# Performance work log

Measured on AMD Instinct MI355X. Metric: run time of the kernel, lower is better.

The kernel has to match this reference:

```python
import jax, jax.numpy as jnp
import numpy as np

B, S, D = 4, 2048, 1024
H = 16
DK = D // H  # 64


def setup_inputs() -> dict:
    key = jax.random.key(0)
    k1, k2, k3 = jax.random.split(key, 3)
    std_qkv = (2.0 / (D + 3 * D)) ** 0.5
    std_o = (2.0 / (D + D)) ** 0.5
    x = jax.random.normal(k1, (B, S, D), dtype=jnp.float32)
    W_qkv = jax.random.normal(k2, (3 * D, D), dtype=jnp.float32) * std_qkv
    W_o = jax.random.normal(k3, (D, D), dtype=jnp.float32) * std_o
    return {"x": x, "W_qkv": W_qkv, "W_o": W_o}


def reference(x, W_qkv, W_o):
    b, s, d = x.shape
    # qkv projection: [b, s, 3*H*DK]
    qkv = jnp.einsum('bsd,ed->bse', x, W_qkv)
    # rearrange '(c h dk)' -> c, b, h, s, dk
    qkv = qkv.reshape(b, s, 3, H, DK)
    qkv = jnp.transpose(qkv, (2, 0, 3, 1, 4))  # [3, b, h, s, dk]
    q, k, v = qkv[0], qkv[1], qkv[2]
    # scaled dot product attention with causal mask
    scores = jnp.einsum('bhqd,bhkd->bhqk', q, k) / (DK ** 0.5)
    causal = jnp.tril(jnp.ones((s, s), dtype=bool))
    scores = jnp.where(causal, scores, -jnp.inf)
    probs = jax.nn.softmax(scores, axis=-1)
    heads = jnp.einsum('bhqk,bhkd->bhqd', probs, v)
    # merge heads: [b, s, H*DK]
    heads = jnp.transpose(heads, (0, 2, 1, 3)).reshape(b, s, H * DK)
    return jnp.einsum('bse,de->bsd', heads, W_o)
```

## Files before the change

kernel.cpp:

```cpp
#include <hip/hip_runtime.h>
#include <hip/hip_bf16.h>

#define BB 4
#define SS 2048
#define DD 1024
#define HH 16
#define DKK 64

typedef __bf16 bf16x8 __attribute__((ext_vector_type(8)));
typedef float floatx4 __attribute__((ext_vector_type(4)));

#if __has_builtin(__builtin_amdgcn_exp2f)
#define EXP2(x) __builtin_amdgcn_exp2f(x)
#else
#define EXP2(x) exp2f(x)
#endif

__device__ __forceinline__ float b2f(unsigned short u) {
    union { unsigned int i; float f; } c;
    c.i = ((unsigned int)u) << 16;
    return c.f;
}
__device__ __forceinline__ unsigned short f2b(float f) {
    unsigned int i = __float_as_uint(f);
    unsigned int r = (i + 0x7FFFu + ((i >> 16) & 1u)) >> 16;
    return (unsigned short)r;
}
__device__ __forceinline__ unsigned int pkpair(float a, float b) {
    unsigned int ia = (__float_as_uint(a) + 0x8000u) >> 16;
    unsigned int ib = (__float_as_uint(b) + 0x8000u) & 0xffff0000u;
    return ia | ib;
}

__device__ __forceinline__ void gload_lds16(const unsigned short* g,
                                            unsigned short* l) {
    __builtin_amdgcn_global_load_lds(
        (const __attribute__((address_space(1))) unsigned int*)g,
        (__attribute__((address_space(3))) unsigned int*)l, 16, 0, 0);
}

__global__ void cvt_f32_bf16(const float* __restrict__ in,
                             unsigned short* __restrict__ out, int n4) {
    int i = blockIdx.x * blockDim.x + threadIdx.x;
    if (i >= n4) return;
    float4 v = ((const float4*)in)[i];
    ushort4 o;
    o.x = f2b(v.x); o.y = f2b(v.y); o.z = f2b(v.z); o.w = f2b(v.w);
    ((ushort4*)out)[i] = o;
}

template <typename CT>
__global__ void gemm_nt_lds(const unsigned short* __restrict__ A,
                            const unsigned short* __restrict__ B,
                            CT* __restrict__ C, int M, int N, int K) {
    __shared__ unsigned short Alds[128][32];
    __shared__ unsigned short Blds[128][32];

    const int tid  = threadIdx.x;
    const int lane = tid & 63;
    const int w    = tid >> 6;
    const int wm   = (w & 1) * 64;
    const int wn   = (w >> 1) * 64;

    const int m0 = blockIdx.x * 128;
    const int n0 = blockIdx.y * 128;

    const int row16 = lane & 15;
    const int part  = lane >> 4;
    const int rbase = part * 4;

    const int srow = lane >> 2;
    const int scol = (lane & 3) * 8;

    const unsigned short* Ag = A + (size_t)(m0 + w * 16 + srow) * K + scol;
    const unsigned short* Bg = B + (size_t)(n0 + w * 16 + srow) * K + scol;
    unsigned short* Al = &Alds[w * 16][0];
    unsigned short* Bl = &Blds[w * 16][0];
    const size_t rstep = (size_t)64 * K;

    floatx4 acc[4][4] = {};

    for (int k0 = 0; k0 < K; k0 += 32) {
        __syncthreads();
        gload_lds16(Ag + k0,         Al);
        gload_lds16(Ag + rstep + k0, Al + 64 * 32);
        gload_lds16(Bg + k0,         Bl);
        gload_lds16(Bg + rstep + k0, Bl + 64 * 32);
        __syncthreads();

        bf16x8 af[4], bfr[4];
#pragma unroll
        for (int i = 0; i < 4; ++i)
            af[i] = *(const bf16x8*)&Alds[wm + i * 16 + row16][part * 8];
#pragma unroll
        for (int j = 0; j < 4; ++j)
            bfr[j] = *(const bf16x8*)&Blds[wn + j * 16 + row16][part * 8];
#pragma unroll
        for (int i = 0; i < 4; ++i)
#pragma unroll
            for (int j = 0; j < 4; ++j)
                acc[i][j] = __builtin_amdgcn_mfma_f32_16x16x32_bf16(
                    af[i], bfr[j], acc[i][j], 0, 0, 0);
    }

#pragma unroll
    for (int i = 0; i < 4; ++i) {
#pragma unroll
        for (int j = 0; j < 4; ++j) {
            const int row = m0 + wm + i * 16 + rbase;
            const int col = n0 + wn + j * 16 + row16;
#pragma unroll
            for (int r = 0; r < 4; ++r) {
                size_t idx = (size_t)(row + r) * N + col;
                if constexpr (sizeof(CT) == 2) C[idx] = f2b(acc[i][j][r]);
                else                           C[idx] = acc[i][j][r];
            }
        }
    }
}

__global__ void repack_kv(const unsigned short* __restrict__ qkv,
                          unsigned short* __restrict__ Kp,
                          unsigned short* __restrict__ Vt) {
    __shared__ unsigned short Vs[64][72];
    const int st = blockIdx.x, h = blockIdx.y, b = blockIdx.z;
    const int tid = threadIdx.x;
    const size_t base = ((size_t)((b * HH + h) * (SS / 64) + st)) * 4096;

#pragma unroll
    for (int p = 0; p < 2; ++p) {
        const int row = p * 32 + (tid >> 3);
        const int chunk = tid & 7;
        size_t src = (size_t)(b * SS + st * 64 + row) * (3 * DD) +
                     DD + h * DKK + chunk * 8;
        uint4 kv = *(const uint4*)(qkv + src);
        *(uint4*)(Kp + base + (chunk >> 2) * 2048 + row * 32 + (chunk & 3) * 8) = kv;
        uint4 vv = *(const uint4*)(qkv + src + DD);
        *(uint4*)&Vs[row][chunk * 8] = vv;
    }
    __syncthreads();
#pragma unroll
    for (int p = 0; p < 2; ++p) {
        const int dk = p * 32 + (tid >> 3);
        const int s8 = tid & 7;
        union { unsigned short u[8]; uint4 v; } pk;
#pragma unroll
        for (int j = 0; j < 8; ++j) pk.u[j] = Vs[s8 * 8 + j][dk];
        *(uint4*)(Vt + base + (s8 >> 2) * 2048 + dk * 32 + (s8 & 3) * 8) = pk.v;
    }
}

struct StripState {
    bf16x8 qf[2][2];
    floatx4 O[2][4];
    float mrow[2], lrow[2];
    int q0w;
};

__device__ __forceinline__ void strip_init(
    StripState& S, const unsigned short* __restrict__ qkv,
    int b, int h, int q0w, int row16, int part) {
    const float c1 = 0.180336884f;
    S.q0w = q0w;
#pragma unroll
    for (int qt = 0; qt < 2; ++qt) {
        S.mrow[qt] = -1e30f;
        S.lrow[qt] = 0.f;
#pragma unroll
        for (int dt = 0; dt < 4; ++dt) S.O[qt][dt] = floatx4{0, 0, 0, 0};
#pragma unroll
        for (int u = 0; u < 2; ++u) {
            const unsigned short* qp = qkv +
                (size_t)(b * SS + q0w + qt * 16 + row16) * (3 * DD) +
                h * DKK + u * 32 + part * 8;
            union { uint4 r; unsigned short us[8]; } raw;
            raw.r = *(const uint4*)qp;
            union { unsigned short us[8]; bf16x8 v; } sq;
#pragma unroll
            for (int j = 0; j < 8; ++j) sq.us[j] = f2b(b2f(raw.us[j]) * c1);
            S.qf[qt][u] = sq.v;
        }
    }
}

__device__ __forceinline__ void strip_tile(
    StripState& S, int k0, const bf16x8 kf[2][4], const bf16x8 vf[2][4],
    int row16, int part, int rbase) {
#pragma unroll
    for (int qt = 0; qt < 2; ++qt) {
        floatx4 sc[4] = {};
#pragma unroll
        for (int u = 0; u < 2; ++u)
#pragma unroll
            for (int kt = 0; kt < 4; ++kt)
                sc[kt] = __builtin_amdgcn_mfma_f32_16x16x32_bf16(
                    kf[u][kt], S.qf[qt][u], sc[kt], 0, 0, 0);

        const int qa = S.q0w + qt * 16 + row16;
        const bool full = (k0 + 63 <= S.q0w + qt * 16);
        float mx = -1e30f;
#pragma unroll
        for (int kt = 0; kt < 4; ++kt)
#pragma unroll
            for (int r = 0; r < 4; ++r) {
                float s = sc[kt][r];
                if (!full) {
                    int ka = k0 + kt * 16 + rbase + r;
                    s = (ka <= qa) ? s : -1e30f;
                }
                sc[kt][r] = s;
                mx = fmaxf(mx, s);
            }
        mx = fmaxf(mx, __shfl_xor(mx, 16));
        mx = fmaxf(mx, __shfl_xor(mx, 32));
        float mnew = fmaxf(S.mrow[qt], mx);
        float alpha = EXP2(S.mrow[qt] - mnew);

        float ps = 0.f;
        unsigned int pk[4][2];
#pragma unroll
        for (int kt = 0; kt < 4; ++kt) {
            float e0 = EXP2(sc[kt][0] - mnew);
            float e1 = EXP2(sc[kt][1] - mnew);
            float e2 = EXP2(sc[kt][2] - mnew);
            float e3 = EXP2(sc[kt][3] - mnew);
            ps += (e0 + e1) + (e2 + e3);
            pk[kt][0] = pkpair(e0, e1);
            pk[kt][1] = pkpair(e2, e3);
        }
        ps += __shfl_xor(ps, 16);
        ps += __shfl_xor(ps, 32);
        S.lrow[qt] = S.lrow[qt] * alpha + ps;
        S.mrow[qt] = mnew;

#pragma unroll
        for (int dt = 0; dt < 4; ++dt) S.O[qt][dt] *= alpha;

        const int l0 = row16 + ((part & 1) * 2 + 0) * 16;
        const int l1 = row16 + ((part & 1) * 2 + 1) * 16;
        const bool hi = (part >> 1);
#pragma unroll
        for (int u = 0; u < 2; ++u) {
            unsigned int lo00 = (unsigned int)__shfl((int)pk[2 * u][0], l0);
            unsigned int lo01 = (unsigned int)__shfl((int)pk[2 * u][1], l0);
            unsigned int lo10 = (unsigned int)__shfl((int)pk[2 * u][0], l1);
            unsigned int lo11 = (unsigned int)__shfl((int)pk[2 * u][1], l1);
            unsigned int hi00 = (unsigned int)__shfl((int)pk[2 * u + 1][0], l0);
            unsigned int hi01 = (unsigned int)__shfl((int)pk[2 * u + 1][1], l0);
            unsigned int hi10 = (unsigned int)__shfl((int)pk[2 * u + 1][0], l1);
            unsigned int hi11 = (unsigned int)__shfl((int)pk[2 * u + 1][1], l1);
            union { unsigned int u32[4]; bf16x8 v; } P;
            P.u32[0] = hi ? hi00 : lo00;
            P.u32[1] = hi ? hi01 : lo01;
            P.u32[2] = hi ? hi10 : lo10;
            P.u32[3] = hi ? hi11 : lo11;
#pragma unroll
            for (int dt = 0; dt < 4; ++dt)
                S.O[qt][dt] = __builtin_amdgcn_mfma_f32_16x16x32_bf16(
                    vf[u][dt], P.v, S.O[qt][dt], 0, 0, 0);
        }
    }
}

__device__ __forceinline__ void strip_store(
    StripState& S, unsigned short* __restrict__ heads,
    int b, int h, int row16, int rbase) {
#pragma unroll
    for (int qt = 0; qt < 2; ++qt) {
        float inv = 1.f / S.lrow[qt];
#pragma unroll
        for (int dt = 0; dt < 4; ++dt) {
            ushort4 o4;
            o4.x = f2b(S.O[qt][dt][0] * inv);
            o4.y = f2b(S.O[qt][dt][1] * inv);
            o4.z = f2b(S.O[qt][dt][2] * inv);
            o4.w = f2b(S.O[qt][dt][3] * inv);
            size_t base = (size_t)(b * SS + S.q0w + qt * 16 + row16) * DD +
                          h * DKK + dt * 16 + rbase;
            *(ushort4*)&heads[base] = o4;
        }
    }
}

__global__ __launch_bounds__(256, 2) void attn_mfma6(
    const unsigned short* __restrict__ qkv,
    const unsigned short* __restrict__ Kp,
    const unsigned short* __restrict__ Vt,
    unsigned short* __restrict__ heads) {
    const int tid  = threadIdx.x;
    const int lane = tid & 63;
    const int w    = tid >> 6;

    const int bx   = blockIdx.x;
    const int xcd  = bx & 7;
    const int slot = bx >> 3;
    const int pair = xcd * 8 + (slot >> 3);
    const int blk  = slot & 7;
    const int b = pair >> 4, h = pair & 15;

    const int jA = blk * 4 + w;
    const int jB = 63 - jA;
    const int ntA = jA / 2 + 1;
    const int ntB = jB / 2 + 1;

    const int row16 = lane & 15;
    const int part  = lane >> 4;
    const int rbase = part * 4;

    StripState SA, SB;
    strip_init(SA, qkv, b, h, jA * 32, row16, part);
    strip_init(SB, qkv, b, h, jB * 32, row16, part);

    const size_t tb = (size_t)pair * (SS / 64) * 4096;

    for (int t = 0; t < ntB; ++t) {
        const int k0 = t * 64;
        const unsigned short* kbase = Kp + tb + (size_t)t * 4096;
        const unsigned short* vbase = Vt + tb + (size_t)t * 4096;
        bf16x8 kf[2][4], vf[2][4];
#pragma unroll
        for (int u = 0; u < 2; ++u)
#pragma unroll
            for (int i = 0; i < 4; ++i) {
                kf[u][i] = *(const bf16x8*)(kbase + u * 2048 +
                                            (i * 16 + row16) * 32 + part * 8);
                vf[u][i] = *(const bf16x8*)(vbase + u * 2048 +
                                            (i * 16 + row16) * 32 + part * 8);
            }
        strip_tile(SB, k0, kf, vf, row16, part, rbase);
        if (t < ntA) strip_tile(SA, k0, kf, vf, row16, part, rbase);
    }

    strip_store(SA, heads, b, h, row16, rbase);
    strip_store(SB, heads, b, h, row16, rbase);
}

extern "C" void kernel_launch(void* const* d_in, const int* in_sizes, int n_in,
                              void* d_out, int out_size, void* d_ws,
                              size_t ws_size, hipStream_t stream) {
    const float* x    = (const float*)d_in[0];
    const float* Wqkv = (const float*)d_in[1];
    const float* Wo   = (const float*)d_in[2];
    float* out = (float*)d_out;

    const size_t NX  = (size_t)BB * SS * DD;
    const size_t NWQ = (size_t)3 * DD * DD;
    const size_t NWO = (size_t)DD * DD;
    const size_t NKV = (size_t)BB * HH * SS * DKK;

    unsigned short* xb     = (unsigned short*)d_ws;
    unsigned short* wqkvb  = xb + NX;
    unsigned short* wob    = wqkvb + NWQ;
    unsigned short* qkvb   = wob + NWO;
    unsigned short* headsb = qkvb + (size_t)BB * SS * 3 * DD;
    unsigned short* Kp     = headsb + NX;
    unsigned short* Vtp    = Kp + NKV;

    cvt_f32_bf16<<<(int)(NX / 4 / 256), 256, 0, stream>>>(x, xb, (int)(NX / 4));
    cvt_f32_bf16<<<(int)(NWQ / 4 / 256), 256, 0, stream>>>(Wqkv, wqkvb, (int)(NWQ / 4));
    cvt_f32_bf16<<<(int)(NWO / 4 / 256), 256, 0, stream>>>(Wo, wob, (int)(NWO / 4));

    gemm_nt_lds<unsigned short><<<dim3(BB * SS / 128, 3 * DD / 128), 256, 0,
                                  stream>>>(xb, wqkvb, qkvb, BB * SS, 3 * DD, DD);

    repack_kv<<<dim3(SS / 64, HH, BB), 256, 0, stream>>>(qkvb, Kp, Vtp);

    attn_mfma6<<<dim3(512), 256, 0, stream>>>(qkvb, Kp, Vtp, headsb);

    gemm_nt_lds<float><<<dim3(BB * SS / 128, DD / 128), 256, 0, stream>>>(
        headsb, wob, out, BB * SS, DD, DD);
}
```

Before: 267.7 us.

## Shrink attention query strips to 16 rows and double block count

Each wave now handles two 16-row query strips instead of two 32-row strips, so the attention kernel launches 1024 blocks rather than 512 and the launch bounds allow 4 blocks per CU. Register pressure per wave drops, which is meant to raise occupancy and improve load balance across CUs. The cost is that each K/V fragment loaded from global memory now feeds half as many query rows, so K/V read traffic per unit of work doubles.

```diff
diff --git a/kernel.cpp b/kernel.cpp
--- a/kernel.cpp
+++ b/kernel.cpp
@@ -151,9 +151,9 @@
 }
 
 struct StripState {
-    bf16x8 qf[2][2];
-    floatx4 O[2][4];
-    float mrow[2], lrow[2];
+    bf16x8 qf[2];
+    floatx4 O[4];
+    float mrow, lrow;
     int q0w;
 };
 
@@ -162,127 +162,118 @@
     int b, int h, int q0w, int row16, int part) {
     const float c1 = 0.180336884f;
     S.q0w = q0w;
-#pragma unroll
-    for (int qt = 0; qt < 2; ++qt) {
-        S.mrow[qt] = -1e30f;
-        S.lrow[qt] = 0.f;
-#pragma unroll
-        for (int dt = 0; dt < 4; ++dt) S.O[qt][dt] = floatx4{0, 0, 0, 0};
-#pragma unroll
-        for (int u = 0; u < 2; ++u) {
-            const unsigned short* qp = qkv +
-                (size_t)(b * SS + q0w + qt * 16 + row16) * (3 * DD) +
-                h * DKK + u * 32 + part * 8;
-            union { uint4 r; unsigned short us[8]; } raw;
-            raw.r = *(const uint4*)qp;
-            union { unsigned short us[8]; bf16x8 v; } sq;
-#pragma unroll
-            for (int j = 0; j < 8; ++j) sq.us[j] = f2b(b2f(raw.us[j]) * c1);
-            S.qf[qt][u] = sq.v;
-        }
+    S.mrow = -1e30f;
+    S.lrow = 0.f;
+#pragma unroll
+    for (int dt = 0; dt < 4; ++dt) S.O[dt] = floatx4{0, 0, 0, 0};
+#pragma unroll
+    for (int u = 0; u < 2; ++u) {
+        const unsigned short* qp = qkv +
+            (size_t)(b * SS + q0w + row16) * (3 * DD) +
+            h * DKK + u * 32 + part * 8;
+        union { uint4 r; unsigned short us[8]; } raw;
+        raw.r = *(const uint4*)qp;
+        union { unsigned short us[8]; bf16x8 v; } sq;
+#pragma unroll
+        for (int j = 0; j < 8; ++j) sq.us[j] = f2b(b2f(raw.us[j]) * c1);
+        S.qf[u] = sq.v;
     }
 }
 
 __device__ __forceinline__ void strip_tile(
     StripState& S, int k0, const bf16x8 kf[2][4], const bf16x8 vf[2][4],
     int row16, int part, int rbase) {
-#pragma unroll
-    for (int qt = 0; qt < 2; ++qt) {
-        floatx4 sc[4] = {};
-#pragma unroll
-        for (int u = 0; u < 2; ++u)
-#pragma unroll
-            for (int kt = 0; kt < 4; ++kt)
-                sc[kt] = __builtin_amdgcn_mfma_f32_16x16x32_bf16(
-                    kf[u][kt], S.qf[qt][u], sc[kt], 0, 0, 0);
-
-        const int qa = S.q0w + qt * 16 + row16;
-        const bool full = (k0 + 63 <= S.q0w + qt * 16);
-        float mx = -1e30f;
+    floatx4 sc[4] = {};
+#pragma unroll
+    for (int u = 0; u < 2; ++u)
 #pragma unroll
         for (int kt = 0; kt < 4; ++kt)
-#pragma unroll
-            for (int r = 0; r < 4; ++r) {
-                float s = sc[kt][r];
-                if (!full) {
-                    int ka = k0 + kt * 16 + rbase + r;
-                    s = (ka <= qa) ? s : -1e30f;
-                }
-                sc[kt][r] = s;
-                mx = fmaxf(mx, s);
+            sc[kt] = __builtin_amdgcn_mfma_f32_16x16x32_bf16(
+                kf[u][kt], S.qf[u], sc[kt], 0, 0, 0);
+
+    const int qa = S.q0w + row16;
+    const bool full = (k0 + 63 <= S.q0w);
+    float mx = -1e30f;
+#pragma unroll
+    for (int kt = 0; kt < 4; ++kt)
+#pragma unroll
+        for (int r = 0; r < 4; ++r) {
+            float s = sc[kt][r];
+            if (!full) {
+                int ka = k0 + kt * 16 + rbase + r;
+                s = (ka <= qa) ? s : -1e30f;
             }
-        mx = fmaxf(mx, __shfl_xor(mx, 16));
-        mx = fmaxf(mx, __shfl_xor(mx, 32));
-        float mnew = fmaxf(S.mrow[qt], mx);
-        float alpha = EXP2(S.mrow[qt] - mnew);
-
-        float ps = 0.f;
-        unsigned int pk[4][2];
-#pragma unroll
-        for (int kt = 0; kt < 4; ++kt) {
-            float e0 = EXP2(sc[kt][0] - mnew);
-            float e1 = EXP2(sc[kt][1] - mnew);
-            float e2 = EXP2(sc[kt][2] - mnew);
-            float e3 = EXP2(sc[kt][3] - mnew);
-            ps += (e0 + e1) + (e2 + e3);
-            pk[kt][0] = pkpair(e0, e1);
-            pk[kt][1] = pkpair(e2, e3);
+            sc[kt][r] = s;
+            mx = fmaxf(mx, s);
         }
-        ps += __shfl_xor(ps, 16);
-        ps += __shfl_xor(ps, 32);
-        S.lrow[qt] = S.lrow[qt] * alpha + ps;
-        S.mrow[qt] = mnew;
-
-#pragma unroll
-        for (int dt = 0; dt < 4; ++dt) S.O[qt][dt] *= alpha;
-
-        const int l0 = row16 + ((part & 1) * 2 + 0) * 16;
-        const int l1 = row16 + ((part & 1) * 2 + 1) * 16;
-        const bool hi = (part >> 1);
-#pragma unroll
-        for (int u = 0; u < 2; ++u) {
-            unsigned int lo00 = (unsigned int)__shfl((int)pk[2 * u][0], l0);
-            unsigned int lo01 = (unsigned int)__shfl((int)pk[2 * u][1], l0);
-            unsigned int lo10 = (unsigned int)__shfl((int)pk[2 * u][0], l1);
-            unsigned int lo11 = (unsigned int)__shfl((int)pk[2 * u][1], l1);
-            unsigned int hi00 = (unsigned int)__shfl((int)pk[2 * u + 1][0], l0);
-            unsigned int hi01 = (unsigned int)__shfl((int)pk[2 * u + 1][1], l0);
-            unsigned int hi10 = (unsigned int)__shfl((int)pk[2 * u + 1][0], l1);
-            unsigned int hi11 = (unsigned int)__shfl((int)pk[2 * u + 1][1], l1);
-            union { unsigned int u32[4]; bf16x8 v; } P;
-            P.u32[0] = hi ? hi00 : lo00;
-            P.u32[1] = hi ? hi01 : lo01;
-            P.u32[2] = hi ? hi10 : lo10;
-            P.u32[3] = hi ? hi11 : lo11;
-#pragma unroll
-            for (int dt = 0; dt < 4; ++dt)
-                S.O[qt][dt] = __builtin_amdgcn_mfma_f32_16x16x32_bf16(
-                    vf[u][dt], P.v, S.O[qt][dt], 0, 0, 0);
-        }
+    mx = fmaxf(mx, __shfl_xor(mx, 16));
+    mx = fmaxf(mx, __shfl_xor(mx, 32));
+    float mnew = fmaxf(S.mrow, mx);
+    float alpha = EXP2(S.mrow - mnew);
+
+    float ps = 0.f;
+    unsigned int pk[4][2];
+#pragma unroll
+    for (int kt = 0; kt < 4; ++kt) {
+        float e0 = EXP2(sc[kt][0] - mnew);
+        float e1 = EXP2(sc[kt][1] - mnew);
+        float e2 = EXP2(sc[kt][2] - mnew);
+        float e3 = EXP2(sc[kt][3] - mnew);
+        ps += (e0 + e1) + (e2 + e3);
+        pk[kt][0] = pkpair(e0, e1);
+        pk[kt][1] = pkpair(e2, e3);
+    }
+    ps += __shfl_xor(ps, 16);
+    ps += __shfl_xor(ps, 32);
+    S.lrow = S.lrow * alpha + ps;
+    S.mrow = mnew;
+
+#pragma unroll
+    for (int dt = 0; dt < 4; ++dt) S.O[dt] *= alpha;
+
+    const int l0 = row16 + ((part & 1) * 2 + 0) * 16;
+    const int l1 = row16 + ((part & 1) * 2 + 1) * 16;
+    const bool hi = (part >> 1);
+#pragma unroll
+    for (int u = 0; u < 2; ++u) {
+        unsigned int lo00 = (unsigned int)__shfl((int)pk[2 * u][0], l0);
+        unsigned int lo01 = (unsigned int)__shfl((int)pk[2 * u][1], l0);
+        unsigned int lo10 = (unsigned int)__shfl((int)pk[2 * u][0], l1);
+        unsigned int lo11 = (unsigned int)__shfl((int)pk[2 * u][1], l1);
+        unsigned int hi00 = (unsigned int)__shfl((int)pk[2 * u + 1][0], l0);
+        unsigned int hi01 = (unsigned int)__shfl((int)pk[2 * u + 1][1], l0);
+        unsigned int hi10 = (unsigned int)__shfl((int)pk[2 * u + 1][0], l1);
+        unsigned int hi11 = (unsigned int)__shfl((int)pk[2 * u + 1][1], l1);
+        union { unsigned int u32[4]; bf16x8 v; } P;
+        P.u32[0] = hi ? hi00 : lo00;
+        P.u32[1] = hi ? hi01 : lo01;
+        P.u32[2] = hi ? hi10 : lo10;
+        P.u32[3] = hi ? hi11 : lo11;
+#pragma unroll
+        for (int dt = 0; dt < 4; ++dt)
+            S.O[dt] = __builtin_amdgcn_mfma_f32_16x16x32_bf16(
+                vf[u][dt], P.v, S.O[dt], 0, 0, 0);
     }
 }
 
 __device__ __forceinline__ void strip_store(
     StripState& S, unsigned short* __restrict__ heads,
     int b, int h, int row16, int rbase) {
-#pragma unroll
-    for (int qt = 0; qt < 2; ++qt) {
-        float inv = 1.f / S.lrow[qt];
-#pragma unroll
-        for (int dt = 0; dt < 4; ++dt) {
-            ushort4 o4;
-            o4.x = f2b(S.O[qt][dt][0] * inv);
-            o4.y = f2b(S.O[qt][dt][1] * inv);
-            o4.z = f2b(S.O[qt][dt][2] * inv);
-            o4.w = f2b(S.O[qt][dt][3] * inv);
-            size_t base = (size_t)(b * SS + S.q0w + qt * 16 + row16) * DD +
-                          h * DKK + dt * 16 + rbase;
-            *(ushort4*)&heads[base] = o4;
-        }
-    }
-}
-
-__global__ __launch_bounds__(256, 2) void attn_mfma6(
+    float inv = 1.f / S.lrow;
+#pragma unroll
+    for (int dt = 0; dt < 4; ++dt) {
+        ushort4 o4;
+        o4.x = f2b(S.O[dt][0] * inv);
+        o4.y = f2b(S.O[dt][1] * inv);
+        o4.z = f2b(S.O[dt][2] * inv);
+        o4.w = f2b(S.O[dt][3] * inv);
+        size_t base = (size_t)(b * SS + S.q0w + row16) * DD +
+                      h * DKK + dt * 16 + rbase;
+        *(ushort4*)&heads[base] = o4;
+    }
+}
+
+__global__ __launch_bounds__(256, 4) void attn_mfma7(
     const unsigned short* __restrict__ qkv,
     const unsigned short* __restrict__ Kp,
     const unsigned short* __restrict__ Vt,
@@ -294,22 +285,22 @@
     const int bx   = blockIdx.x;
     const int xcd  = bx & 7;
     const int slot = bx >> 3;
-    const int pair = xcd * 8 + (slot >> 3);
-    const int blk  = slot & 7;
+    const int pair = xcd * 8 + (slot >> 4);
+    const int blk  = slot & 15;
     const int b = pair >> 4, h = pair & 15;
 
     const int jA = blk * 4 + w;
-    const int jB = 63 - jA;
-    const int ntA = jA / 2 + 1;
-    const int ntB = jB / 2 + 1;
+    const int jB = 127 - jA;
+    const int ntA = jA / 4 + 1;
+    const int ntB = jB / 4 + 1;
 
     const int row16 = lane & 15;
     const int part  = lane >> 4;
     const int rbase = part * 4;
 
     StripState SA, SB;
-    strip_init(SA, qkv, b, h, jA * 32, row16, part);
-    strip_init(SB, qkv, b, h, jB * 32, row16, part);
+    strip_init(SA, qkv, b, h, jA * 16, row16, part);
+    strip_init(SB, qkv, b, h, jB * 16, row16, part);
 
     const size_t tb = (size_t)pair * (SS / 64) * 4096;
 
@@ -365,7 +356,7 @@
 
     repack_kv<<<dim3(SS / 64, HH, BB), 256, 0, stream>>>(qkvb, Kp, Vtp);
 
-    attn_mfma6<<<dim3(512), 256, 0, stream>>>(qkvb, Kp, Vtp, headsb);
+    attn_mfma7<<<dim3(1024), 256, 0, stream>>>(qkvb, Kp, Vtp, headsb);
 
     gemm_nt_lds<float><<<dim3(BB * SS / 128, DD / 128), 256, 0, stream>>>(
         headsb, wob, out, BB * SS, DD, DD);
```

New measurement: 439.7 us. +64.2%, slower.

## Rewrite GEMM with double-buffered 256x128 tiles, swizzled LDS and phased MFMA

Applied to the files above, without the earlier changes.

The projection GEMM kernel now uses 256x128 block tiles with 8 waves and BK=64. It double-buffers LDS through async global-to-LDS loads, waiting on partial vmcnt so the next tile streams in while MFMAs run. LDS columns are XOR-swizzled to avoid bank conflicts, and the MFMA work is split into barrier-separated phases with raised priority. This trades more LDS per block (96KB dynamic, set via a one-time attribute) and extra barriers for better load/compute overlap and reuse.

```diff
diff --git a/kernel.cpp b/kernel.cpp
--- a/kernel.cpp
+++ b/kernel.cpp
@@ -50,58 +50,110 @@
 }
 
 template <typename CT>
-__global__ void gemm_nt_lds(const unsigned short* __restrict__ A,
-                            const unsigned short* __restrict__ B,
-                            CT* __restrict__ C, int M, int N, int K) {
-    __shared__ unsigned short Alds[128][32];
-    __shared__ unsigned short Blds[128][32];
+__global__ __launch_bounds__(512, 2) void gemm_nt_8ph(
+    const unsigned short* __restrict__ A,
+    const unsigned short* __restrict__ B,
+    CT* __restrict__ C, int M, int N, int K) {
+    extern __shared__ unsigned short lds[];
+    unsigned short* At = lds;
+    unsigned short* Bt = lds + 2 * 256 * 64;
 
     const int tid  = threadIdx.x;
     const int lane = tid & 63;
     const int w    = tid >> 6;
-    const int wm   = (w & 1) * 64;
-    const int wn   = (w >> 1) * 64;
-
-    const int m0 = blockIdx.x * 128;
+    const int wm   = (w >> 1) * 64;
+    const int wn   = (w & 1) * 64;
+
+    const int m0 = blockIdx.x * 256;
     const int n0 = blockIdx.y * 128;
 
     const int row16 = lane & 15;
     const int part  = lane >> 4;
     const int rbase = part * 4;
 
-    const int srow = lane >> 2;
-    const int scol = (lane & 3) * 8;
-
-    const unsigned short* Ag = A + (size_t)(m0 + w * 16 + srow) * K + scol;
-    const unsigned short* Bg = B + (size_t)(n0 + w * 16 + srow) * K + scol;
-    unsigned short* Al = &Alds[w * 16][0];
-    unsigned short* Bl = &Blds[w * 16][0];
-    const size_t rstep = (size_t)64 * K;
-
+    const int srow  = lane >> 3;
+    const int scol  = ((lane & 7) * 8) ^ ((srow & 6) << 2);
+
+    const unsigned short* Ag = A + (size_t)(m0 + srow) * K + scol;
+    const unsigned short* Bg = B + (size_t)(n0 + srow) * K + scol;
+
+    const int NT = K >> 6;
     floatx4 acc[4][4] = {};
 
-    for (int k0 = 0; k0 < K; k0 += 32) {
-        __syncthreads();
-        gload_lds16(Ag + k0,         Al);
-        gload_lds16(Ag + rstep + k0, Al + 64 * 32);
-        gload_lds16(Bg + k0,         Bl);
-        gload_lds16(Bg + rstep + k0, Bl + 64 * 32);
-        __syncthreads();
-
-        bf16x8 af[4], bfr[4];
-#pragma unroll
-        for (int i = 0; i < 4; ++i)
-            af[i] = *(const bf16x8*)&Alds[wm + i * 16 + row16][part * 8];
+    const int shr = (row16 & 6) << 2;
+
+#define STAGE(t, bb)                                                        \
+    {                                                                       \
+        const size_t koff = (size_t)(t) * 64;                               \
+        _Pragma("unroll") for (int a = 0; a < 4; ++a) {                     \
+            const int rb = (w * 4 + a) * 8;                                 \
+            gload_lds16(Ag + (size_t)rb * K + koff,                         \
+                        At + (bb) * 16384 + rb * 64);                       \
+        }                                                                   \
+        _Pragma("unroll") for (int bi = 0; bi < 2; ++bi) {                  \
+            const int rb = (w * 2 + bi) * 8;                                \
+            gload_lds16(Bg + (size_t)rb * K + koff,                         \
+                        Bt + (bb) * 8192 + rb * 64);                        \
+        }                                                                   \
+    }
+
+    STAGE(0, 0);
+
+    for (int t = 0; t < NT; ++t) {
+        const int cur = t & 1;
+        if (t + 1 < NT) {
+            STAGE(t + 1, cur ^ 1);
+            asm volatile("s_waitcnt vmcnt(6)" ::: "memory");
+        } else {
+            asm volatile("s_waitcnt vmcnt(0)" ::: "memory");
+        }
+        __builtin_amdgcn_sched_barrier(0);
+        __builtin_amdgcn_s_barrier();
+
+        const unsigned short* Ab = At + cur * 16384;
+        const unsigned short* Bb = Bt + cur * 8192;
+
+        bf16x8 bf[4][2];
 #pragma unroll
         for (int j = 0; j < 4; ++j)
-            bfr[j] = *(const bf16x8*)&Blds[wn + j * 16 + row16][part * 8];
-#pragma unroll
-        for (int i = 0; i < 4; ++i)
-#pragma unroll
-            for (int j = 0; j < 4; ++j)
-                acc[i][j] = __builtin_amdgcn_mfma_f32_16x16x32_bf16(
-                    af[i], bfr[j], acc[i][j], 0, 0, 0);
-    }
+#pragma unroll
+            for (int u = 0; u < 2; ++u)
+                bf[j][u] = *(const bf16x8*)(Bb + (wn + j * 16 + row16) * 64 +
+                                            ((u * 32 + part * 8) ^ shr));
+
+#pragma unroll
+        for (int qm = 0; qm < 2; ++qm) {
+            bf16x8 af[2][2];
+#pragma unroll
+            for (int i = 0; i < 2; ++i)
+#pragma unroll
+                for (int u = 0; u < 2; ++u)
+                    af[i][u] = *(const bf16x8*)(
+                        Ab + (wm + (qm * 2 + i) * 16 + row16) * 64 +
+                        ((u * 32 + part * 8) ^ shr));
+#pragma unroll
+            for (int qn = 0; qn < 2; ++qn) {
+                __builtin_amdgcn_s_barrier();
+                asm volatile("s_waitcnt lgkmcnt(0)" ::: "memory");
+                __builtin_amdgcn_sched_barrier(0);
+                __builtin_amdgcn_s_setprio(1);
+#pragma unroll
+                for (int i = 0; i < 2; ++i)
+#pragma unroll
+                    for (int j = 0; j < 2; ++j)
+#pragma unroll
+                        for (int u = 0; u < 2; ++u)
+                            acc[qm * 2 + i][qn * 2 + j] =
+                                __builtin_amdgcn_mfma_f32_16x16x32_bf16(
+                                    af[i][u], bf[qn * 2 + j][u],
+                                    acc[qm * 2 + i][qn * 2 + j], 0, 0, 0);
+                __builtin_amdgcn_s_setprio(0);
+                __builtin_amdgcn_sched_barrier(0);
+                __builtin_amdgcn_s_barrier();
+            }
+        }
+    }
+#undef STAGE
 
 #pragma unroll
     for (int i = 0; i < 4; ++i) {
@@ -356,17 +408,29 @@
     unsigned short* Kp     = headsb + NX;
     unsigned short* Vtp    = Kp + NKV;
 
+    static bool attr_done = false;
+    if (!attr_done) {
+        hipFuncSetAttribute(
+            reinterpret_cast<const void*>(&gemm_nt_8ph<unsigned short>),
+            hipFuncAttributeMaxDynamicSharedMemorySize, 98304);
+        hipFuncSetAttribute(
+            reinterpret_cast<const void*>(&gemm_nt_8ph<float>),
+            hipFuncAttributeMaxDynamicSharedMemorySize, 98304);
+        attr_done = true;
+    }
+
     cvt_f32_bf16<<<(int)(NX / 4 / 256), 256, 0, stream>>>(x, xb, (int)(NX / 4));
     cvt_f32_bf16<<<(int)(NWQ / 4 / 256), 256, 0, stream>>>(Wqkv, wqkvb, (int)(NWQ / 4));
     cvt_f32_bf16<<<(int)(NWO / 4 / 256), 256, 0, stream>>>(Wo, wob, (int)(NWO / 4));
 
-    gemm_nt_lds<unsigned short><<<dim3(BB * SS / 128, 3 * DD / 128), 256, 0,
-                                  stream>>>(xb, wqkvb, qkvb, BB * SS, 3 * DD, DD);
+    gemm_nt_8ph<unsigned short><<<dim3(BB * SS / 256, 3 * DD / 128), 512,
+                                  98304, stream>>>(xb, wqkvb, qkvb,
+                                                   BB * SS, 3 * DD, DD);
 
     repack_kv<<<dim3(SS / 64, HH, BB), 256, 0, stream>>>(qkvb, Kp, Vtp);
 
     attn_mfma6<<<dim3(512), 256, 0, stream>>>(qkvb, Kp, Vtp, headsb);
 
-    gemm_nt_lds<float><<<dim3(BB * SS / 128, DD / 128), 256, 0, stream>>>(
+    gemm_nt_8ph<float><<<dim3(BB * SS / 256, DD / 128), 512, 98304, stream>>>(
         headsb, wob, out, BB * SS, DD, DD);
 }
```

Result: slower. 277.6 us (+3.7%).
